# Optimization experiments

Measured on AMD Instinct MI355X. Metric: run time of the kernel, lower is better.

The kernel has to match this reference:

```python
import jax, jax.numpy as jnp
import numpy as np

B, N, K = 32, 64, 128          # batch, atoms per cell, channel width (128x0e + 128x1o)
R_MAX = 5.0
NUM_BESSEL = 8
P_CUT = 5                       # num_polynomial_cutoff
AVG_NEIGH = 16.0                # avg_num_neighbors
H_MLP = 512                     # hidden_dimensions_size, n_hidden_dimensions = 2
FEAT = 5 * K                    # ((num_interactions-1)*4 + 1) * 128 = 640


def silu(x):
    return x * jax.nn.sigmoid(x)


def _bessel_cutoff(r, mask):
    # Bessel radial basis * polynomial cutoff (MACE), masked on valid edges.
    n = jnp.arange(1, NUM_BESSEL + 1, dtype=r.dtype)
    rb = jnp.sqrt(2.0 / R_MAX) * jnp.sin(n * (jnp.pi / R_MAX) * r[..., None]) / r[..., None]
    u = r / R_MAX
    p = float(P_CUT)
    fc = 1.0 - 0.5 * (p + 1) * (p + 2) * u**P_CUT + p * (p + 2) * u**(P_CUT + 1) - 0.5 * p * (p + 1) * u**(P_CUT + 2)
    fc = fc * (u < 1.0)
    return rb * (fc * mask)[..., None]


def _sph(uvec):
    # Real spherical harmonics l=0,1,2 (component normalization), uvec: unit edge vectors.
    x, y, z = uvec[..., 0], uvec[..., 1], uvec[..., 2]
    s3, s5, s15 = 3.0**0.5, 5.0**0.5, 15.0**0.5
    Y0 = jnp.ones_like(x)[..., None]
    Y1 = jnp.stack([s3 * x, s3 * y, s3 * z], -1)
    Y2 = jnp.stack([s15 * x * y, s15 * y * z, 0.5 * s5 * (3 * z * z - 1.0),
                    s15 * x * z, 0.5 * s15 * (x * x - y * y)], -1)
    return Y0, Y1, Y2


def _radial_mlp(x, w0, b0, w1, b1, w2, b2, w3, b3):
    h = silu(x @ w0 + b0)
    h = silu(h @ w1 + b1)
    h = silu(h @ w2 + b2)
    return h @ w3 + b3


def setup_inputs() -> dict:
    key = jax.random.key(0)
    ks = jax.random.split(key, 32)
    f32 = jnp.float32

    def lin(k, fan_in, shape):
        return (jax.random.normal(k, shape, dtype=f32) / np.sqrt(fan_in)).astype(f32)

    inp = {
        "noisy_relative_positions": jax.random.uniform(ks[0], (B, N, 3), dtype=f32),
        "time": jax.random.uniform(ks[1], (B, 1), dtype=f32),
        "unit_cell": (11.0 * jnp.eye(3, dtype=f32) + 0.3 * jax.random.uniform(ks[2], (B, 3, 3), dtype=f32)),
        "w_embed": lin(ks[3], 1, (K,)),
        # interaction 1 radial MLP: 8 -> 64 -> 64 -> 64 -> 3*K (weights for l=0,1,2 paths)
        "r1_w0": lin(ks[4], NUM_BESSEL, (NUM_BESSEL, 64)), "r1_b0": jnp.zeros((64,), f32),
        "r1_w1": lin(ks[5], 64, (64, 64)), "r1_b1": jnp.zeros((64,), f32),
        "r1_w2": lin(ks[6], 64, (64, 64)), "r1_b2": jnp.zeros((64,), f32),
        "r1_w3": lin(ks[7], 64, (64, 3 * K)), "r1_b3": jnp.zeros((3 * K,), f32),
        "mix1_l0": lin(ks[8], K, (K, K)),
        "mix1_l1": lin(ks[9], K, (K, K)),
        "mix1_l2": lin(ks[10], K, (K, K)),
        # interaction 2 radial MLP: 8 -> 64 -> 64 -> 64 -> 2*K (paths 0e x 0e -> 0e, 1o x 1o -> 0e)
        "r2_w0": lin(ks[11], NUM_BESSEL, (NUM_BESSEL, 64)), "r2_b0": jnp.zeros((64,), f32),
        "r2_w1": lin(ks[12], 64, (64, 64)), "r2_b1": jnp.zeros((64,), f32),
        "r2_w2": lin(ks[13], 64, (64, 64)), "r2_b2": jnp.zeros((64,), f32),
        "r2_w3": lin(ks[14], 64, (64, 2 * K)), "r2_b3": jnp.zeros((2 * K,), f32),
        "mix2": lin(ks[15], K, (K, K)),
        # readout MLP: 641 -> 512 -> 512 -> 3
        "mlp_w0": lin(ks[16], FEAT + 1, (FEAT + 1, H_MLP)), "mlp_b0": jnp.zeros((H_MLP,), f32),
        "mlp_w1": lin(ks[17], H_MLP, (H_MLP, H_MLP)), "mlp_b1": jnp.zeros((H_MLP,), f32),
        "mlp_w2": lin(ks[18], H_MLP, (H_MLP, 3)), "mlp_b2": jnp.zeros((3,), f32),
    }
    return inp


def reference(noisy_relative_positions, time, unit_cell, w_embed,
              r1_w0, r1_b0, r1_w1, r1_b1, r1_w2, r1_b2, r1_w3, r1_b3,
              mix1_l0, mix1_l1, mix1_l2,
              r2_w0, r2_b0, r2_w1, r2_b1, r2_w2, r2_b2, r2_w3, r2_b3, mix2,
              mlp_w0, mlp_b0, mlp_w1, mlp_b1, mlp_w2, mlp_b2):
    frac = noisy_relative_positions                      # [B,N,3] fractional
    d = frac[:, :, None, :] - frac[:, None, :, :]        # [B,N,N,3]
    d = d - jnp.round(d)                                 # minimum-image PBC
    dc = jnp.einsum('bijc,bcd->bijd', d, unit_cell)      # cartesian displacements
    r = jnp.sqrt(jnp.maximum(jnp.sum(dc * dc, -1), 1e-12))
    mask = (r < R_MAX) & (~jnp.eye(N, dtype=bool))[None]
    r_safe = jnp.where(mask, r, 1.0)
    uvec = dc / r_safe[..., None] * mask[..., None]      # unit edge vectors (0 off-edge)

    rad = _bessel_cutoff(r_safe, mask)                   # [B,N,N,8]
    Y0, Y1, Y2 = _sph(uvec)                              # [B,N,N,1|3|5]

    h0 = jnp.broadcast_to(w_embed, (B, N, K))            # element embedding (single species)

    # ---- interaction 1: radial-weighted tensor product h_j (x) Y_l, scatter over j ----
    we = _radial_mlp(rad, r1_w0, r1_b0, r1_w1, r1_b1, r1_w2, r1_b2, r1_w3, r1_b3)
    we = we.reshape(B, N, N, 3, K) * mask[..., None, None]
    hj = h0[:, None, :, :]                               # sender features [B,1,N,K]
    msg0 = jnp.einsum('bijk,bijm->bimk', we[..., 0, :] * hj, Y0)[:, :, 0] / AVG_NEIGH  # [B,N,K]
    msg1 = jnp.einsum('bijk,bijm->bimk', we[..., 1, :] * hj, Y1) / AVG_NEIGH           # [B,N,3,K]
    msg2 = jnp.einsum('bijk,bijm->bimk', we[..., 2, :] * hj, Y2) / AVG_NEIGH           # [B,N,5,K]

    s1 = msg0 @ mix1_l0 + jnp.sum(msg2 * msg2, axis=2) @ mix1_l2   # scalars [B,N,K]
    v1 = jnp.einsum('bimk,kc->bimc', msg1, mix1_l1)                # vectors [B,N,3,K]
    h1 = silu(s1)

    # ---- interaction 2: scalar output from 0e x 0e and 1o x 1o -> 0e paths ----
    we2 = _radial_mlp(rad, r2_w0, r2_b0, r2_w1, r2_b1, r2_w2, r2_b2, r2_w3, r2_b3)
    we2 = we2.reshape(B, N, N, 2, K) * mask[..., None, None]
    msg_a = jnp.sum(we2[..., 0, :] * h1[:, None, :, :], axis=2)    # [B,N,K]
    inv = jnp.einsum('bijm,bjmk->bijk', Y1, v1)                    # Y1 . v1_j invariant
    msg_b = jnp.sum(we2[..., 1, :] * inv, axis=2)
    s2 = ((msg_a + msg_b) / AVG_NEIGH) @ mix2                      # [B,N,K]

    # node_feats: layer1 full irreps (128x0e + 128x1o -> 512) + layer2 scalars (128) = 640
    node_feats = jnp.concatenate([s1, v1.reshape(B, N, 3 * K), s2], axis=-1)

    t = jnp.broadcast_to(time[:, None, :], (B, N, 1))
    x = jnp.concatenate([node_feats, t], axis=-1)                  # [B,N,641]
    x = jax.nn.relu(x @ mlp_w0 + mlp_b0)
    x = jax.nn.relu(x @ mlp_w1 + mlp_b1)
    return x @ mlp_w2 + mlp_b2                                     # [B,N,3]
```

## Files before the change

kernel.cpp:

```cpp
#include <hip/hip_runtime.h>
#include <math.h>

#define B_ 32
#define N_ 64
#define K_ 128
#define NPAIR (B_*N_*N_)

typedef __attribute__((ext_vector_type(8))) short short8;
typedef __attribute__((ext_vector_type(8))) __bf16 bf16x8;
typedef __attribute__((ext_vector_type(4))) float floatx4;

__device__ __forceinline__ float silu_f(float x) {
    return x / (1.0f + expf(-x));
}
__device__ __forceinline__ float4 ld4(const float* p) { return *(const float4*)p; }

__device__ __forceinline__ short f2bf(float x) {
    union { float f; unsigned u; } v; v.f = x;
    unsigned r = (v.u + 0x7FFFu + ((v.u >> 16) & 1u)) >> 16;
    return (short)r;
}
__device__ __forceinline__ float bf2f(short s) {
    union { unsigned u; float f; } v;
    v.u = ((unsigned)(unsigned short)s) << 16;
    return v.f;
}
__device__ __forceinline__ bf16x8 ld_frag(const short* p) {
    short8 r = *(const short8*)p;
    return __builtin_bit_cast(bf16x8, r);
}

__global__ __launch_bounds__(256) void prep_kernel(
    const float* __restrict__ r1w1, const float* __restrict__ r1w2,
    const float* __restrict__ r2w1, const float* __restrict__ r2w2,
    const float* __restrict__ r2w3, const float* __restrict__ mw0,
    const float* __restrict__ mw1, short* __restrict__ dst)
{
    int idx = blockIdx.x * 256 + threadIdx.x;
    if (idx >= 655360) return;
    short v;
    if (idx < 4096) {
        int h = idx >> 6, k = idx & 63; v = f2bf(r1w1[k*64 + h]);
    } else if (idx < 8192) {
        int i = idx - 4096; int h = i >> 6, k = i & 63; v = f2bf(r1w2[k*64 + h]);
    } else if (idx < 12288) {
        int i = idx - 8192; int h = i >> 6, k = i & 63; v = f2bf(r2w1[k*64 + h]);
    } else if (idx < 16384) {
        int i = idx - 12288; int h = i >> 6, k = i & 63; v = f2bf(r2w2[k*64 + h]);
    } else if (idx < 32768) {
        int i = idx - 16384; int col = i >> 6, h = i & 63; v = f2bf(r2w3[h*256 + col]);
    } else if (idx < 393216) {
        int i = idx - 32768; int n = i / 704, k = i - n*704;
        v = (k < 641) ? f2bf(mw0[(size_t)k*512 + n]) : (short)0;
    } else {
        int i = idx - 393216; int n = i >> 9, k = i & 511;
        v = f2bf(mw1[(size_t)k*512 + n]);
    }
    dst[idx] = v;
}

__global__ __launch_bounds__(256) void geom_kernel(
    const float* __restrict__ pos, const float* __restrict__ cell,
    float* __restrict__ rad, float* __restrict__ Y1, float* __restrict__ Y2,
    float* __restrict__ maskf)
{
    int p = blockIdx.x * 256 + threadIdx.x;
    if (p >= NPAIR) return;
    int b = p >> 12;
    int ij = p & 4095;
    int i = ij >> 6, j = ij & 63;
    const float* pi = pos + (size_t)(b*N_ + i)*3;
    const float* pj = pos + (size_t)(b*N_ + j)*3;
    float d0 = pi[0]-pj[0], d1 = pi[1]-pj[1], d2 = pi[2]-pj[2];
    d0 -= rintf(d0); d1 -= rintf(d1); d2 -= rintf(d2);
    const float* C = cell + b*9;
    float dc0 = d0*C[0] + d1*C[3] + d2*C[6];
    float dc1 = d0*C[1] + d1*C[4] + d2*C[7];
    float dc2 = d0*C[2] + d1*C[5] + d2*C[8];
    float r2 = fmaxf(dc0*dc0 + dc1*dc1 + dc2*dc2, 1e-12f);
    float r = sqrtf(r2);
    bool m = (r < 5.0f) && (i != j);
    float mf = m ? 1.0f : 0.0f;
    float rs = m ? r : 1.0f;
    float inv_rs = 1.0f / rs;
    float x = dc0*inv_rs*mf, y = dc1*inv_rs*mf, z = dc2*inv_rs*mf;
    float u = r * 0.2f;
    float u2 = u*u, u4 = u2*u2, u5 = u4*u;
    float fc = 1.0f - 21.0f*u5 + 35.0f*u5*u - 15.0f*u5*u2;
    fc = (u < 1.0f) ? fc : 0.0f;
    float pref = 0.6324555320336759f * inv_rs * (fc * mf);
    float w = 0.6283185307179586f * rs;
    #pragma unroll
    for (int n = 1; n <= 8; n++)
        rad[(size_t)p*8 + (n-1)] = pref * sinf((float)n * w);
    const float s3  = 1.7320508075688772f;
    const float s5  = 2.23606797749979f;
    const float s15 = 3.872983346207417f;
    float* y1 = Y1 + (size_t)p*3;
    y1[0] = s3*x; y1[1] = s3*y; y1[2] = s3*z;
    float* y2 = Y2 + (size_t)p*5;
    y2[0] = s15*x*y;
    y2[1] = s15*y*z;
    y2[2] = 0.5f*s5*(3.0f*z*z - 1.0f);
    y2[3] = s15*x*z;
    y2[4] = 0.5f*s15*(x*x - y*y);
    maskf[p] = mf;
}

__device__ __forceinline__ void mfma_layer(
    const short* __restrict__ src, const short* __restrict__ WT,
    const float* __restrict__ bias, short* __restrict__ dst,
    int wv, int qd, int nn)
{
    floatx4 acc[4];
    #pragma unroll
    for (int tt = 0; tt < 4; tt++) acc[tt] = (floatx4){0.f, 0.f, 0.f, 0.f};
    #pragma unroll
    for (int ks = 0; ks < 64; ks += 32) {
        bf16x8 a = ld_frag(&src[(wv*16 + nn)*72 + ks + qd*8]);
        #pragma unroll
        for (int tt = 0; tt < 4; tt++) {
            bf16x8 b = ld_frag(&WT[(tt*16 + nn)*64 + ks + qd*8]);
            acc[tt] = __builtin_amdgcn_mfma_f32_16x16x32_bf16(a, b, acc[tt], 0, 0, 0);
        }
    }
    #pragma unroll
    for (int tt = 0; tt < 4; tt++) {
        int col = tt*16 + nn;
        float bv = bias[col];
        #pragma unroll
        for (int i = 0; i < 4; i++) {
            int row = wv*16 + qd*4 + i;
            dst[row*72 + col] = f2bf(silu_f(acc[tt][i] + bv));
        }
    }
}

__global__ __launch_bounds__(256) void pass1_kernel(
    const float* __restrict__ rad, const float* __restrict__ Y1g,
    const float* __restrict__ Y2g, const float* __restrict__ maskg,
    const float* __restrict__ wemb,
    const float* __restrict__ w0, const float* __restrict__ b0,
    const short* __restrict__ w1T, const float* __restrict__ b1,
    const short* __restrict__ w2T, const float* __restrict__ b2,
    const float* __restrict__ w3, const float* __restrict__ b3,
    const float* __restrict__ l0, const float* __restrict__ l1,
    const float* __restrict__ l2, const float* __restrict__ timeg,
    float* __restrict__ h1g, float* __restrict__ v1g, short* __restrict__ featsb)
{
    __shared__ float rad_s[512];
    __shared__ short actA[64*72];
    __shared__ short actB[64*72];
    __shared__ float Ym[9*64];
    __shared__ float G[9*64];
    __shared__ float SY[9];
    __shared__ float msg[9*128];
    __shared__ float q_s[128];
    int t = threadIdx.x;
    int wv = t >> 6, lane = t & 63, qd = lane >> 4, nn = lane & 15;
    int node = blockIdx.x;
    int b = node >> 6;
    size_t pbase = (size_t)node * 64;

    for (int idx = t; idx < 512; idx += 256) rad_s[idx] = rad[pbase*8 + idx];
    if (t < 64) {
        int j = t;
        float mf = maskg[pbase + j];
        Ym[j] = mf;
        #pragma unroll
        for (int m = 0; m < 3; m++) Ym[(1+m)*64 + j] = Y1g[(pbase+j)*3 + m] * mf;
        #pragma unroll
        for (int m = 0; m < 5; m++) Ym[(4+m)*64 + j] = Y2g[(pbase+j)*5 + m] * mf;
    }
    __syncthreads();

    for (int idx = t; idx < 4096; idx += 256) {
        int j = idx >> 6, h = idx & 63;
        float acc = b0[h];
        #pragma unroll
        for (int c = 0; c < 8; c++) acc += rad_s[j*8+c] * w0[c*64+h];
        actA[j*72 + h] = f2bf(silu_f(acc));
    }
    __syncthreads();
    mfma_layer(actA, w1T, b1, actB, wv, qd, nn);
    __syncthreads();
    mfma_layer(actB, w2T, b2, actA, wv, qd, nn);
    __syncthreads();

    if (t < 9) {
        float acc = 0.f;
        for (int j = 0; j < 64; j++) acc += Ym[t*64 + j];
        SY[t] = acc;
    }
    for (int idx = t; idx < 576; idx += 256) {
        int m = idx >> 6, h = idx & 63;
        float acc = 0.f;
        #pragma unroll 8
        for (int j = 0; j < 64; j++) acc += Ym[m*64 + j] * bf2f(actA[j*72 + h]);
        G[m*64 + h] = acc;
    }
    __syncthreads();

    for (int idx = t; idx < 1152; idx += 256) {
        int m = idx >> 7, k = idx & 127;
        int c = (m == 0) ? 0 : ((m < 4) ? 1 : 2);
        int col = c*128 + k;
        float acc = SY[m] * b3[col];
        #pragma unroll 8
        for (int h = 0; h < 64; h++) acc += G[m*64 + h] * w3[h*384 + col];
        msg[m*128 + k] = acc * wemb[k] * 0.0625f;
    }
    __syncthreads();

    if (t < 128) {
        int k = t;
        float acc = 0.f;
        #pragma unroll
        for (int m = 4; m < 9; m++) { float v = msg[m*128 + k]; acc += v*v; }
        q_s[k] = acc;
    }
    __syncthreads();

    for (int idx = t; idx < 512; idx += 256) {
        if (idx < 128) {
            int c = idx;
            float acc = 0.f;
            for (int k = 0; k < 128; k++)
                acc += msg[k]*l0[k*128 + c] + q_s[k]*l2[k*128 + c];
            featsb[(size_t)node*704 + c] = f2bf(acc);
            h1g[(size_t)node*128 + c] = silu_f(acc);
        } else {
            int vi = idx - 128;
            int m = vi >> 7, c = vi & 127;
            float acc = 0.f;
            for (int k = 0; k < 128; k++) acc += msg[(1+m)*128 + k]*l1[k*128 + c];
            v1g[(size_t)node*384 + m*128 + c] = acc;
            featsb[(size_t)node*704 + 128 + m*128 + c] = f2bf(acc);
        }
    }
    if (t == 0) featsb[(size_t)node*704 + 640] = f2bf(timeg[b]);
    if (t < 63) featsb[(size_t)node*704 + 641 + t] = 0;
}

__global__ __launch_bounds__(256) void pass2_kernel(
    const float* __restrict__ rad, const float* __restrict__ Y1g,
    const float* __restrict__ maskg,
    const float* __restrict__ w0, const float* __restrict__ b0,
    const short* __restrict__ w1T, const float* __restrict__ b1,
    const short* __restrict__ w2T, const float* __restrict__ b2,
    const short* __restrict__ w3T, const float* __restrict__ b3,
    const float* __restrict__ mix2,
    const float* __restrict__ h1g, const float* __restrict__ v1g,
    short* __restrict__ featsb)
{
    __shared__ float rad_s[512];
    __shared__ short actA[64*72];
    __shared__ short actB[64*72];
    __shared__ float Y1s[64*4];
    __shared__ float mask_s[64];
    __shared__ float msgab[128];
    int t = threadIdx.x;
    int wv = t >> 6, lane = t & 63, qd = lane >> 4, nn = lane & 15;
    int node = blockIdx.x;
    int b = node >> 6;
    size_t pbase = (size_t)node * 64;

    for (int idx = t; idx < 512; idx += 256) rad_s[idx] = rad[pbase*8 + idx];
    if (t < 64) {
        mask_s[t] = maskg[pbase + t];
        #pragma unroll
        for (int m = 0; m < 3; m++) Y1s[t*4 + m] = Y1g[(pbase+t)*3 + m];
    }
    if (t < 128) msgab[t] = 0.f;
    __syncthreads();

    for (int idx = t; idx < 4096; idx += 256) {
        int j = idx >> 6, h = idx & 63;
        float acc = b0[h];
        #pragma unroll
        for (int c = 0; c < 8; c++) acc += rad_s[j*8+c] * w0[c*64+h];
        actA[j*72 + h] = f2bf(silu_f(acc));
    }
    __syncthreads();
    mfma_layer(actA, w1T, b1, actB, wv, qd, nn);
    __syncthreads();
    mfma_layer(actB, w2T, b2, actA, wv, qd, nn);
    __syncthreads();

    for (int g = 0; g < 4; g++) {
        floatx4 acc[4];
        #pragma unroll
        for (int tt = 0; tt < 4; tt++) acc[tt] = (floatx4){0.f, 0.f, 0.f, 0.f};
        #pragma unroll
        for (int ks = 0; ks < 64; ks += 32) {
            bf16x8 a = ld_frag(&actA[(wv*16 + nn)*72 + ks + qd*8]);
            #pragma unroll
            for (int tt = 0; tt < 4; tt++) {
                int col0 = g*64 + tt*16;
                bf16x8 bb = ld_frag(&w3T[(col0 + nn)*64 + ks + qd*8]);
                acc[tt] = __builtin_amdgcn_mfma_f32_16x16x32_bf16(a, bb, acc[tt], 0, 0, 0);
            }
        }
        #pragma unroll
        for (int tt = 0; tt < 4; tt++) {
            int col = g*64 + tt*16 + nn;
            float bias = b3[col];
            int k = col & 127;
            float p = 0.f;
            if (col < 128) {
                #pragma unroll
                for (int i = 0; i < 4; i++) {
                    int j = wv*16 + qd*4 + i;
                    float we = (acc[tt][i] + bias) * mask_s[j];
                    p += we * h1g[((size_t)b*64 + j)*128 + k];
                }
            } else {
                #pragma unroll
                for (int i = 0; i < 4; i++) {
                    int j = wv*16 + qd*4 + i;
                    float we = (acc[tt][i] + bias) * mask_s[j];
                    const float* vb = &v1g[((size_t)b*64 + j)*384 + k];
                    float inv = Y1s[j*4+0]*vb[0] + Y1s[j*4+1]*vb[128] + Y1s[j*4+2]*vb[256];
                    p += we * inv;
                }
            }
            p += __shfl_xor(p, 16);
            p += __shfl_xor(p, 32);
            if (qd == 0) atomicAdd(&msgab[k], p);
        }
    }
    __syncthreads();

    if (t < 128) {
        int c = t;
        float acc = 0.f;
        for (int k = 0; k < 128; k++) acc += msgab[k] * mix2[k*128 + c];
        featsb[(size_t)node*704 + 512 + c] = f2bf(acc * 0.0625f);
    }
}

__global__ __launch_bounds__(256) void gemm_mfma_kernel(
    const short* __restrict__ A, int lda,
    const short* __restrict__ BT, int ldb, int K,
    const float* __restrict__ bias, short* __restrict__ Cout, int ldo)
{
    __shared__ short As[64*72];
    __shared__ short Bs[64*72];
    int t = threadIdx.x;
    int wv = t >> 6, lane = t & 63, qd = lane >> 4, nn = lane & 15;
    int m0 = blockIdx.x * 64, n0 = blockIdx.y * 64;
    floatx4 acc[4];
    #pragma unroll
    for (int tt = 0; tt < 4; tt++) acc[tt] = (floatx4){0.f, 0.f, 0.f, 0.f};

    for (int kc = 0; kc < K; kc += 64) {
        for (int s = t; s < 512; s += 256) {
            int j = s >> 3, kk = (s & 7) * 8;
            *(uint4*)&As[j*72 + kk] = *(const uint4*)&A[(size_t)(m0 + j)*lda + kc + kk];
            *(uint4*)&Bs[j*72 + kk] = *(const uint4*)&BT[(size_t)(n0 + j)*ldb + kc + kk];
        }
        __syncthreads();
        #pragma unroll
        for (int ks = 0; ks < 64; ks += 32) {
            bf16x8 a = ld_frag(&As[(wv*16 + nn)*72 + ks + qd*8]);
            #pragma unroll
            for (int tt = 0; tt < 4; tt++) {
                bf16x8 bb = ld_frag(&Bs[(tt*16 + nn)*72 + ks + qd*8]);
                acc[tt] = __builtin_amdgcn_mfma_f32_16x16x32_bf16(a, bb, acc[tt], 0, 0, 0);
            }
        }
        __syncthreads();
    }
    #pragma unroll
    for (int tt = 0; tt < 4; tt++) {
        int n = n0 + tt*16 + nn;
        float bv = bias[n];
        #pragma unroll
        for (int i = 0; i < 4; i++) {
            int m = m0 + wv*16 + qd*4 + i;
            Cout[(size_t)m*ldo + n] = f2bf(fmaxf(acc[tt][i] + bv, 0.f));
        }
    }
}

__global__ __launch_bounds__(64) void final3_kernel(
    const short* __restrict__ H, const float* __restrict__ w2,
    const float* __restrict__ b2, float* __restrict__ out)
{
    int node = blockIdx.x, lane = threadIdx.x;
    float a0 = 0.f, a1 = 0.f, a2 = 0.f;
    #pragma unroll
    for (int r = 0; r < 8; r++) {
        int k = r*64 + lane;
        float h = bf2f(H[(size_t)node*512 + k]);
        a0 += h * w2[k*3 + 0];
        a1 += h * w2[k*3 + 1];
        a2 += h * w2[k*3 + 2];
    }
    #pragma unroll
    for (int off = 32; off > 0; off >>= 1) {
        a0 += __shfl_down(a0, off);
        a1 += __shfl_down(a1, off);
        a2 += __shfl_down(a2, off);
    }
    if (lane == 0) {
        out[(size_t)node*3 + 0] = a0 + b2[0];
        out[(size_t)node*3 + 1] = a1 + b2[1];
        out[(size_t)node*3 + 2] = a2 + b2[2];
    }
}

extern "C" void kernel_launch(void* const* d_in, const int* in_sizes, int n_in,
                              void* d_out, int out_size, void* d_ws, size_t ws_size,
                              hipStream_t stream) {
    const float* pos   = (const float*)d_in[0];
    const float* timeg = (const float*)d_in[1];
    const float* cell  = (const float*)d_in[2];
    const float* wemb  = (const float*)d_in[3];
    const float* r1w0  = (const float*)d_in[4];
    const float* r1b0  = (const float*)d_in[5];
    const float* r1w1  = (const float*)d_in[6];
    const float* r1b1  = (const float*)d_in[7];
    const float* r1w2  = (const float*)d_in[8];
    const float* r1b2  = (const float*)d_in[9];
    const float* r1w3  = (const float*)d_in[10];
    const float* r1b3  = (const float*)d_in[11];
    const float* l0    = (const float*)d_in[12];
    const float* l1    = (const float*)d_in[13];
    const float* l2    = (const float*)d_in[14];
    const float* r2w0  = (const float*)d_in[15];
    const float* r2b0  = (const float*)d_in[16];
    const float* r2w1  = (const float*)d_in[17];
    const float* r2b1  = (const float*)d_in[18];
    const float* r2w2  = (const float*)d_in[19];
    const float* r2b2  = (const float*)d_in[20];
    const float* r2w3  = (const float*)d_in[21];
    const float* r2b3  = (const float*)d_in[22];
    const float* mix2  = (const float*)d_in[23];
    const float* mw0   = (const float*)d_in[24];
    const float* mb0   = (const float*)d_in[25];
    const float* mw1   = (const float*)d_in[26];
    const float* mb1   = (const float*)d_in[27];
    const float* mw2   = (const float*)d_in[28];
    const float* mb2   = (const float*)d_in[29];

    float* ws    = (float*)d_ws;
    float* rad   = ws;
    float* Y1    = rad   + (size_t)NPAIR*8;
    float* Y2    = Y1    + (size_t)NPAIR*3;
    float* maskf = Y2    + (size_t)NPAIR*5;
    float* h1    = maskf + (size_t)NPAIR;
    float* v1    = h1    + (size_t)B_*N_*K_;
    short* featsb = (short*)(v1 + (size_t)B_*N_*3*K_);
    short* prep  = featsb + (size_t)2048*704;
    short* w1T_1 = prep;
    short* w2T_1 = prep + 4096;
    short* w1T_2 = prep + 8192;
    short* w2T_2 = prep + 12288;
    short* w3T_2 = prep + 16384;
    short* wT0   = prep + 32768;
    short* wT1   = prep + 393216;
    short* h0bb = (short*)rad;
    short* h1bb = (short*)Y2;

    prep_kernel<<<(655360 + 255)/256, 256, 0, stream>>>(
        r1w1, r1w2, r2w1, r2w2, r2w3, mw0, mw1, prep);
    geom_kernel<<<NPAIR/256, 256, 0, stream>>>(pos, cell, rad, Y1, Y2, maskf);
    pass1_kernel<<<B_*N_, 256, 0, stream>>>(rad, Y1, Y2, maskf, wemb,
        r1w0, r1b0, w1T_1, r1b1, w2T_1, r1b2, r1w3, r1b3, l0, l1, l2, timeg,
        h1, v1, featsb);
    pass2_kernel<<<B_*N_, 256, 0, stream>>>(rad, Y1, maskf,
        r2w0, r2b0, w1T_2, r2b1, w2T_2, r2b2, w3T_2, r2b3, mix2, h1, v1, featsb);
    dim3 g0(32, 8);
    gemm_mfma_kernel<<<g0, 256, 0, stream>>>(featsb, 704, wT0, 704, 704, mb0, h0bb, 512);
    gemm_mfma_kernel<<<g0, 256, 0, stream>>>(h0bb, 512, wT1, 512, 512, mb1, h1bb, 512);
    final3_kernel<<<B_*N_, 64, 0, stream>>>(h1bb, mw2, mb2, (float*)d_out);
}
```

Measured before the change: 286.0 us.

## Move remaining radial-MLP and mixing stages of both interaction passes onto bf16 MFMA

The first radial layer, the Y·h contraction, the w3 projection and the l0/l1/l2 channel mixing in pass1 now run as bf16 MFMA tiles instead of scalar FP32 loops. pass2 stages h1 and the Y1·v1 invariant into shared memory as bf16 rather than re-reading global memory per MFMA output. The prep kernel adds transposed bf16 copies of w0, w3 (with wemb and 1/16 folded in) and the stacked mixing weights, and the geometry kernel computes the Bessel sines with a Chebyshev recurrence and vector stores. Shared memory is packed into one aliased pool. The extra bf16 rounding of intermediates adds numerical error.

```diff
diff --git a/kernel.cpp b/kernel.cpp
--- a/kernel.cpp
+++ b/kernel.cpp
@@ -31,30 +31,50 @@
 }
 
 __global__ __launch_bounds__(256) void prep_kernel(
-    const float* __restrict__ r1w1, const float* __restrict__ r1w2,
-    const float* __restrict__ r2w1, const float* __restrict__ r2w2,
-    const float* __restrict__ r2w3, const float* __restrict__ mw0,
-    const float* __restrict__ mw1, short* __restrict__ dst)
+    const float* __restrict__ r1w0, const float* __restrict__ r1w1,
+    const float* __restrict__ r1w2, const float* __restrict__ r1w3,
+    const float* __restrict__ r2w0, const float* __restrict__ r2w1,
+    const float* __restrict__ r2w2, const float* __restrict__ r2w3,
+    const float* __restrict__ mw0, const float* __restrict__ mw1,
+    const float* __restrict__ wemb,
+    const float* __restrict__ l0, const float* __restrict__ l1,
+    const float* __restrict__ l2, short* __restrict__ dst)
 {
     int idx = blockIdx.x * 256 + threadIdx.x;
-    if (idx >= 655360) return;
+    if (idx >= 733184) return;
     short v;
     if (idx < 4096) {
-        int h = idx >> 6, k = idx & 63; v = f2bf(r1w1[k*64 + h]);
+        int n = idx >> 6, k = idx & 63; v = f2bf(r1w1[k*64 + n]);
     } else if (idx < 8192) {
-        int i = idx - 4096; int h = i >> 6, k = i & 63; v = f2bf(r1w2[k*64 + h]);
+        int i = idx - 4096; int n = i >> 6, k = i & 63; v = f2bf(r1w2[k*64 + n]);
     } else if (idx < 12288) {
-        int i = idx - 8192; int h = i >> 6, k = i & 63; v = f2bf(r2w1[k*64 + h]);
+        int i = idx - 8192; int n = i >> 6, k = i & 63; v = f2bf(r2w1[k*64 + n]);
     } else if (idx < 16384) {
-        int i = idx - 12288; int h = i >> 6, k = i & 63; v = f2bf(r2w2[k*64 + h]);
+        int i = idx - 12288; int n = i >> 6, k = i & 63; v = f2bf(r2w2[k*64 + n]);
     } else if (idx < 32768) {
         int i = idx - 16384; int col = i >> 6, h = i & 63; v = f2bf(r2w3[h*256 + col]);
     } else if (idx < 393216) {
         int i = idx - 32768; int n = i / 704, k = i - n*704;
         v = (k < 641) ? f2bf(mw0[(size_t)k*512 + n]) : (short)0;
-    } else {
+    } else if (idx < 655360) {
         int i = idx - 393216; int n = i >> 9, k = i & 511;
         v = f2bf(mw1[(size_t)k*512 + n]);
+    } else if (idx < 657408) {
+        int i = idx - 655360; int n = i >> 5, k = i & 31;
+        v = (k < 8) ? f2bf(r1w0[k*64 + n]) : (short)0;
+    } else if (idx < 659456) {
+        int i = idx - 657408; int n = i >> 5, k = i & 31;
+        v = (k < 8) ? f2bf(r2w0[k*64 + n]) : (short)0;
+    } else if (idx < 684032) {
+        int i = idx - 659456; int col = i >> 6, h = i & 63;
+        v = f2bf(r1w3[h*384 + col] * wemb[col & 127] * 0.0625f);
+    } else {
+        int i = idx - 684032; int n = i / 384, k = i - n*384;
+        float f;
+        if (k < 128)       f = l0[k*128 + n];
+        else if (k < 256)  f = l2[(k-128)*128 + n];
+        else               f = l1[(k-256)*128 + n];
+        v = f2bf(f);
     }
     dst[idx] = v;
 }
@@ -90,9 +110,20 @@
     fc = (u < 1.0f) ? fc : 0.0f;
     float pref = 0.6324555320336759f * inv_rs * (fc * mf);
     float w = 0.6283185307179586f * rs;
-    #pragma unroll
-    for (int n = 1; n <= 8; n++)
-        rad[(size_t)p*8 + (n-1)] = pref * sinf((float)n * w);
+    float sw = sinf(w), cw = cosf(w);
+    float c2 = 2.0f * cw;
+    float rr[8];
+    float sp = 0.f, s = sw;
+    #pragma unroll
+    for (int n = 0; n < 8; n++) {
+        rr[n] = pref * s;
+        float ns = c2*s - sp;
+        sp = s; s = ns;
+    }
+    float4 v0 = {rr[0], rr[1], rr[2], rr[3]};
+    float4 v1 = {rr[4], rr[5], rr[6], rr[7]};
+    *(float4*)&rad[(size_t)p*8]     = v0;
+    *(float4*)&rad[(size_t)p*8 + 4] = v1;
     const float s3  = 1.7320508075688772f;
     const float s5  = 2.23606797749979f;
     const float s15 = 3.872983346207417f;
@@ -107,7 +138,8 @@
     maskf[p] = mf;
 }
 
-__device__ __forceinline__ void mfma_layer(
+template<bool TRANSPOSE_OUT>
+__device__ __forceinline__ void mfma_layer_t(
     const short* __restrict__ src, const short* __restrict__ WT,
     const float* __restrict__ bias, short* __restrict__ dst,
     int wv, int qd, int nn)
@@ -131,7 +163,30 @@
         #pragma unroll
         for (int i = 0; i < 4; i++) {
             int row = wv*16 + qd*4 + i;
-            dst[row*72 + col] = f2bf(silu_f(acc[tt][i] + bv));
+            short val = f2bf(silu_f(acc[tt][i] + bv));
+            if (TRANSPOSE_OUT) dst[col*72 + row] = val;
+            else               dst[row*72 + col] = val;
+        }
+    }
+}
+
+__device__ __forceinline__ void mfma_layer0(
+    const short* __restrict__ radB, const short* __restrict__ w0T,
+    const float* __restrict__ bias, short* __restrict__ dst,
+    int wv, int qd, int nn)
+{
+    bf16x8 a = ld_frag(&radB[(wv*16 + nn)*40 + qd*8]);
+    #pragma unroll
+    for (int tt = 0; tt < 4; tt++) {
+        floatx4 acc = (floatx4){0.f, 0.f, 0.f, 0.f};
+        bf16x8 b = ld_frag(&w0T[(tt*16 + nn)*32 + qd*8]);
+        acc = __builtin_amdgcn_mfma_f32_16x16x32_bf16(a, b, acc, 0, 0, 0);
+        int col = tt*16 + nn;
+        float bv = bias[col];
+        #pragma unroll
+        for (int i = 0; i < 4; i++) {
+            int row = wv*16 + qd*4 + i;
+            dst[row*72 + col] = f2bf(silu_f(acc[i] + bv));
         }
     }
 }
@@ -140,102 +195,141 @@
     const float* __restrict__ rad, const float* __restrict__ Y1g,
     const float* __restrict__ Y2g, const float* __restrict__ maskg,
     const float* __restrict__ wemb,
-    const float* __restrict__ w0, const float* __restrict__ b0,
+    const short* __restrict__ w0T, const float* __restrict__ b0,
     const short* __restrict__ w1T, const float* __restrict__ b1,
     const short* __restrict__ w2T, const float* __restrict__ b2,
-    const float* __restrict__ w3, const float* __restrict__ b3,
-    const float* __restrict__ l0, const float* __restrict__ l1,
-    const float* __restrict__ l2, const float* __restrict__ timeg,
+    const short* __restrict__ w3T, const float* __restrict__ b3,
+    const short* __restrict__ lT, const float* __restrict__ timeg,
     float* __restrict__ h1g, float* __restrict__ v1g, short* __restrict__ featsb)
 {
-    __shared__ float rad_s[512];
-    __shared__ short actA[64*72];
-    __shared__ short actB[64*72];
-    __shared__ float Ym[9*64];
-    __shared__ float G[9*64];
-    __shared__ float SY[9];
-    __shared__ float msg[9*128];
-    __shared__ float q_s[128];
+    __shared__ __align__(16) char pool[32832];
+    short* radB = (short*)pool;
+    short* hcT  = (short*)pool;
+    short* actA = (short*)(pool + 9216);
+    short* actB = (short*)(pool + 18432);
+    short* A2   = (short*)(pool + 9216);
+    float* msgF = (float*)(pool + 21760);
+    short* YmB  = (short*)(pool + 27648);
+    short* GB   = (short*)(pool + 29952);
+    float* qF   = (float*)(pool + 32256);
+    float* SY   = (float*)(pool + 32768);
+
     int t = threadIdx.x;
     int wv = t >> 6, lane = t & 63, qd = lane >> 4, nn = lane & 15;
     int node = blockIdx.x;
     int b = node >> 6;
     size_t pbase = (size_t)node * 64;
 
-    for (int idx = t; idx < 512; idx += 256) rad_s[idx] = rad[pbase*8 + idx];
+    for (int idx = t; idx < 2560; idx += 256) {
+        int j = idx / 40, c = idx - j*40;
+        radB[idx] = (c < 8) ? f2bf(rad[pbase*8 + j*8 + c]) : (short)0;
+    }
+    for (int idx = t; idx < 1152; idx += 256) YmB[idx] = 0;
+    __syncthreads();
+
     if (t < 64) {
         int j = t;
         float mf = maskg[pbase + j];
-        Ym[j] = mf;
-        #pragma unroll
-        for (int m = 0; m < 3; m++) Ym[(1+m)*64 + j] = Y1g[(pbase+j)*3 + m] * mf;
-        #pragma unroll
-        for (int m = 0; m < 5; m++) Ym[(4+m)*64 + j] = Y2g[(pbase+j)*5 + m] * mf;
-    }
-    __syncthreads();
-
-    for (int idx = t; idx < 4096; idx += 256) {
-        int j = idx >> 6, h = idx & 63;
-        float acc = b0[h];
-        #pragma unroll
-        for (int c = 0; c < 8; c++) acc += rad_s[j*8+c] * w0[c*64+h];
-        actA[j*72 + h] = f2bf(silu_f(acc));
-    }
-    __syncthreads();
-    mfma_layer(actA, w1T, b1, actB, wv, qd, nn);
-    __syncthreads();
-    mfma_layer(actB, w2T, b2, actA, wv, qd, nn);
-    __syncthreads();
-
-    if (t < 9) {
+        YmB[j] = f2bf(mf);
+        #pragma unroll
+        for (int m = 0; m < 3; m++) YmB[(1+m)*72 + j] = f2bf(Y1g[(pbase+j)*3 + m] * mf);
+        #pragma unroll
+        for (int m = 0; m < 5; m++) YmB[(4+m)*72 + j] = f2bf(Y2g[(pbase+j)*5 + m] * mf);
+    }
+    mfma_layer0(radB, w0T, b0, actA, wv, qd, nn);
+    __syncthreads();
+
+    mfma_layer_t<false>(actA, w1T, b1, actB, wv, qd, nn);
+    __syncthreads();
+    mfma_layer_t<true >(actB, w2T, b2, hcT,  wv, qd, nn);
+    __syncthreads();
+
+    if (t < 16) {
         float acc = 0.f;
-        for (int j = 0; j < 64; j++) acc += Ym[t*64 + j];
+        if (t < 9) for (int j = 0; j < 64; j++) acc += bf2f(YmB[t*72 + j]);
         SY[t] = acc;
     }
-    for (int idx = t; idx < 576; idx += 256) {
-        int m = idx >> 6, h = idx & 63;
+    {
+        floatx4 accG = (floatx4){0.f, 0.f, 0.f, 0.f};
+        #pragma unroll
+        for (int ks = 0; ks < 64; ks += 32) {
+            bf16x8 a = ld_frag(&YmB[nn*72 + ks + qd*8]);
+            bf16x8 bfr = ld_frag(&hcT[(wv*16 + nn)*72 + ks + qd*8]);
+            accG = __builtin_amdgcn_mfma_f32_16x16x32_bf16(a, bfr, accG, 0, 0, 0);
+        }
+        #pragma unroll
+        for (int i = 0; i < 4; i++)
+            GB[(qd*4 + i)*72 + wv*16 + nn] = f2bf(accG[i]);
+    }
+    __syncthreads();
+
+    {
+        bf16x8 a0f = ld_frag(&GB[nn*72 + 0  + qd*8]);
+        bf16x8 a1f = ld_frag(&GB[nn*72 + 32 + qd*8]);
+        #pragma unroll
+        for (int tl = 0; tl < 6; tl++) {
+            int col0 = (wv*6 + tl)*16;
+            floatx4 acc = (floatx4){0.f, 0.f, 0.f, 0.f};
+            bf16x8 b0f = ld_frag(&w3T[(col0 + nn)*64 + 0  + qd*8]);
+            bf16x8 b1f = ld_frag(&w3T[(col0 + nn)*64 + 32 + qd*8]);
+            acc = __builtin_amdgcn_mfma_f32_16x16x32_bf16(a0f, b0f, acc, 0, 0, 0);
+            acc = __builtin_amdgcn_mfma_f32_16x16x32_bf16(a1f, b1f, acc, 0, 0, 0);
+            int col = col0 + nn;
+            int csec = col >> 7, k = col & 127;
+            #pragma unroll
+            for (int i = 0; i < 4; i++) {
+                int m = qd*4 + i;
+                bool valid = (csec == 0) ? (m == 0)
+                           : (csec == 1) ? (m >= 1 && m <= 3)
+                                         : (m >= 4 && m <= 8);
+                if (valid)
+                    msgF[m*128 + k] = acc[i] + SY[m]*b3[col]*wemb[k]*0.0625f;
+            }
+        }
+    }
+    __syncthreads();
+
+    if (t < 128) {
         float acc = 0.f;
-        #pragma unroll 8
-        for (int j = 0; j < 64; j++) acc += Ym[m*64 + j] * bf2f(actA[j*72 + h]);
-        G[m*64 + h] = acc;
-    }
-    __syncthreads();
-
-    for (int idx = t; idx < 1152; idx += 256) {
-        int m = idx >> 7, k = idx & 127;
-        int c = (m == 0) ? 0 : ((m < 4) ? 1 : 2);
-        int col = c*128 + k;
-        float acc = SY[m] * b3[col];
-        #pragma unroll 8
-        for (int h = 0; h < 64; h++) acc += G[m*64 + h] * w3[h*384 + col];
-        msg[m*128 + k] = acc * wemb[k] * 0.0625f;
-    }
-    __syncthreads();
-
-    if (t < 128) {
-        int k = t;
-        float acc = 0.f;
-        #pragma unroll
-        for (int m = 4; m < 9; m++) { float v = msg[m*128 + k]; acc += v*v; }
-        q_s[k] = acc;
-    }
-    __syncthreads();
-
-    for (int idx = t; idx < 512; idx += 256) {
-        if (idx < 128) {
-            int c = idx;
-            float acc = 0.f;
-            for (int k = 0; k < 128; k++)
-                acc += msg[k]*l0[k*128 + c] + q_s[k]*l2[k*128 + c];
-            featsb[(size_t)node*704 + c] = f2bf(acc);
-            h1g[(size_t)node*128 + c] = silu_f(acc);
-        } else {
-            int vi = idx - 128;
-            int m = vi >> 7, c = vi & 127;
-            float acc = 0.f;
-            for (int k = 0; k < 128; k++) acc += msg[(1+m)*128 + k]*l1[k*128 + c];
-            v1g[(size_t)node*384 + m*128 + c] = acc;
-            featsb[(size_t)node*704 + 128 + m*128 + c] = f2bf(acc);
+        #pragma unroll
+        for (int m = 4; m < 9; m++) { float v = msgF[m*128 + t]; acc += v*v; }
+        qF[t] = acc;
+    }
+    __syncthreads();
+
+    for (int idx = t; idx < 6272; idx += 256) A2[idx] = 0;
+    __syncthreads();
+    {
+        int idx = t;
+        A2[idx] = (idx < 128) ? f2bf(msgF[idx]) : f2bf(qF[idx - 128]);
+        if (t < 128) {
+            #pragma unroll
+            for (int m = 1; m <= 3; m++)
+                A2[m*392 + 256 + t] = f2bf(msgF[m*128 + t]);
+        }
+    }
+    __syncthreads();
+
+    #pragma unroll
+    for (int tt = 0; tt < 2; tt++) {
+        int col = (wv*2 + tt)*16 + nn;
+        floatx4 acc = (floatx4){0.f, 0.f, 0.f, 0.f};
+        #pragma unroll
+        for (int ks = 0; ks < 384; ks += 32) {
+            bf16x8 a = ld_frag(&A2[nn*392 + ks + qd*8]);
+            bf16x8 bfr = ld_frag(&lT[(size_t)col*384 + ks + qd*8]);
+            acc = __builtin_amdgcn_mfma_f32_16x16x32_bf16(a, bfr, acc, 0, 0, 0);
+        }
+        if (qd == 0) {
+            float s1 = acc[0];
+            featsb[(size_t)node*704 + col] = f2bf(s1);
+            h1g[(size_t)node*128 + col] = silu_f(s1);
+            #pragma unroll
+            for (int i = 1; i < 4; i++) {
+                float v = acc[i];
+                v1g[(size_t)node*384 + (i-1)*128 + col] = v;
+                featsb[(size_t)node*704 + 128 + (i-1)*128 + col] = f2bf(v);
+            }
         }
     }
     if (t == 0) featsb[(size_t)node*704 + 640] = f2bf(timeg[b]);
@@ -245,7 +339,7 @@
 __global__ __launch_bounds__(256) void pass2_kernel(
     const float* __restrict__ rad, const float* __restrict__ Y1g,
     const float* __restrict__ maskg,
-    const float* __restrict__ w0, const float* __restrict__ b0,
+    const short* __restrict__ w0T, const float* __restrict__ b0,
     const short* __restrict__ w1T, const float* __restrict__ b1,
     const short* __restrict__ w2T, const float* __restrict__ b2,
     const short* __restrict__ w3T, const float* __restrict__ b3,
@@ -253,19 +347,27 @@
     const float* __restrict__ h1g, const float* __restrict__ v1g,
     short* __restrict__ featsb)
 {
-    __shared__ float rad_s[512];
-    __shared__ short actA[64*72];
-    __shared__ short actB[64*72];
-    __shared__ float Y1s[64*4];
-    __shared__ float mask_s[64];
-    __shared__ float msgab[128];
+    __shared__ __align__(16) char pool[46848];
+    short* radB  = (short*)pool;
+    short* hc    = (short*)pool;
+    short* actA  = (short*)(pool + 9216);
+    short* actB  = (short*)(pool + 18432);
+    short* h1B   = (short*)(pool + 9216);
+    short* invB  = (short*)(pool + 27648);
+    float* Y1s   = (float*)(pool + 45056);
+    float* mask_s= (float*)(pool + 46080);
+    float* msgab = (float*)(pool + 46336);
+
     int t = threadIdx.x;
     int wv = t >> 6, lane = t & 63, qd = lane >> 4, nn = lane & 15;
     int node = blockIdx.x;
     int b = node >> 6;
     size_t pbase = (size_t)node * 64;
 
-    for (int idx = t; idx < 512; idx += 256) rad_s[idx] = rad[pbase*8 + idx];
+    for (int idx = t; idx < 2560; idx += 256) {
+        int j = idx / 40, c = idx - j*40;
+        radB[idx] = (c < 8) ? f2bf(rad[pbase*8 + j*8 + c]) : (short)0;
+    }
     if (t < 64) {
         mask_s[t] = maskg[pbase + t];
         #pragma unroll
@@ -274,68 +376,67 @@
     if (t < 128) msgab[t] = 0.f;
     __syncthreads();
 
-    for (int idx = t; idx < 4096; idx += 256) {
-        int j = idx >> 6, h = idx & 63;
-        float acc = b0[h];
-        #pragma unroll
-        for (int c = 0; c < 8; c++) acc += rad_s[j*8+c] * w0[c*64+h];
-        actA[j*72 + h] = f2bf(silu_f(acc));
-    }
-    __syncthreads();
-    mfma_layer(actA, w1T, b1, actB, wv, qd, nn);
-    __syncthreads();
-    mfma_layer(actB, w2T, b2, actA, wv, qd, nn);
-    __syncthreads();
-
-    for (int g = 0; g < 4; g++) {
-        floatx4 acc[4];
-        #pragma unroll
-        for (int tt = 0; tt < 4; tt++) acc[tt] = (floatx4){0.f, 0.f, 0.f, 0.f};
-        #pragma unroll
-        for (int ks = 0; ks < 64; ks += 32) {
-            bf16x8 a = ld_frag(&actA[(wv*16 + nn)*72 + ks + qd*8]);
+    mfma_layer0(radB, w0T, b0, actA, wv, qd, nn);
+    __syncthreads();
+    mfma_layer_t<false>(actA, w1T, b1, actB, wv, qd, nn);
+    __syncthreads();
+    mfma_layer_t<false>(actB, w2T, b2, hc, wv, qd, nn);
+    __syncthreads();
+
+    for (int idx = t; idx < 2048; idx += 256) {
+        int j = idx >> 5, kq = (idx & 31)*4;
+        size_t gj = (size_t)b*64 + j;
+        float4 hv = ld4(&h1g[gj*128 + kq]);
+        h1B[j*136 + kq + 0] = f2bf(hv.x);
+        h1B[j*136 + kq + 1] = f2bf(hv.y);
+        h1B[j*136 + kq + 2] = f2bf(hv.z);
+        h1B[j*136 + kq + 3] = f2bf(hv.w);
+        const float* vb = &v1g[gj*384 + kq];
+        float4 vx = ld4(vb), vy = ld4(vb + 128), vz = ld4(vb + 256);
+        float yx = Y1s[j*4+0], yy = Y1s[j*4+1], yz = Y1s[j*4+2];
+        invB[j*136 + kq + 0] = f2bf(yx*vx.x + yy*vy.x + yz*vz.x);
+        invB[j*136 + kq + 1] = f2bf(yx*vx.y + yy*vy.y + yz*vz.y);
+        invB[j*136 + kq + 2] = f2bf(yx*vx.z + yy*vy.z + yz*vz.z);
+        invB[j*136 + kq + 3] = f2bf(yx*vx.w + yy*vy.w + yz*vz.w);
+    }
+    __syncthreads();
+
+    {
+        bf16x8 aA = ld_frag(&hc[(wv*16 + nn)*72 + 0  + qd*8]);
+        bf16x8 aB = ld_frag(&hc[(wv*16 + nn)*72 + 32 + qd*8]);
+        #pragma unroll
+        for (int g = 0; g < 4; g++) {
             #pragma unroll
             for (int tt = 0; tt < 4; tt++) {
                 int col0 = g*64 + tt*16;
-                bf16x8 bb = ld_frag(&w3T[(col0 + nn)*64 + ks + qd*8]);
-                acc[tt] = __builtin_amdgcn_mfma_f32_16x16x32_bf16(a, bb, acc[tt], 0, 0, 0);
-            }
-        }
-        #pragma unroll
-        for (int tt = 0; tt < 4; tt++) {
-            int col = g*64 + tt*16 + nn;
-            float bias = b3[col];
-            int k = col & 127;
-            float p = 0.f;
-            if (col < 128) {
+                floatx4 acc = (floatx4){0.f, 0.f, 0.f, 0.f};
+                bf16x8 b0f = ld_frag(&w3T[(col0 + nn)*64 + 0  + qd*8]);
+                bf16x8 b1f = ld_frag(&w3T[(col0 + nn)*64 + 32 + qd*8]);
+                acc = __builtin_amdgcn_mfma_f32_16x16x32_bf16(aA, b0f, acc, 0, 0, 0);
+                acc = __builtin_amdgcn_mfma_f32_16x16x32_bf16(aB, b1f, acc, 0, 0, 0);
+                int col = col0 + nn;
+                int k = col & 127;
+                float bias = b3[col];
+                const short* src = (col < 128) ? h1B : invB;
+                float p = 0.f;
                 #pragma unroll
                 for (int i = 0; i < 4; i++) {
                     int j = wv*16 + qd*4 + i;
-                    float we = (acc[tt][i] + bias) * mask_s[j];
-                    p += we * h1g[((size_t)b*64 + j)*128 + k];
+                    float we = (acc[i] + bias) * mask_s[j];
+                    p += we * bf2f(src[j*136 + k]);
                 }
-            } else {
-                #pragma unroll
-                for (int i = 0; i < 4; i++) {
-                    int j = wv*16 + qd*4 + i;
-                    float we = (acc[tt][i] + bias) * mask_s[j];
-                    const float* vb = &v1g[((size_t)b*64 + j)*384 + k];
-                    float inv = Y1s[j*4+0]*vb[0] + Y1s[j*4+1]*vb[128] + Y1s[j*4+2]*vb[256];
-                    p += we * inv;
-                }
+                p += __shfl_xor(p, 16);
+                p += __shfl_xor(p, 32);
+                if (qd == 0) atomicAdd(&msgab[k], p);
             }
-            p += __shfl_xor(p, 16);
-            p += __shfl_xor(p, 32);
-            if (qd == 0) atomicAdd(&msgab[k], p);
         }
     }
     __syncthreads();
 
     if (t < 128) {
-        int c = t;
         float acc = 0.f;
-        for (int k = 0; k < 128; k++) acc += msgab[k] * mix2[k*128 + c];
-        featsb[(size_t)node*704 + 512 + c] = f2bf(acc * 0.0625f);
+        for (int k = 0; k < 128; k++) acc += msgab[k] * mix2[k*128 + t];
+        featsb[(size_t)node*704 + 512 + t] = f2bf(acc * 0.0625f);
     }
 }
 
@@ -460,17 +561,22 @@
     short* w3T_2 = prep + 16384;
     short* wT0   = prep + 32768;
     short* wT1   = prep + 393216;
+    short* w0T_1 = prep + 655360;
+    short* w0T_2 = prep + 657408;
+    short* w3T_1 = prep + 659456;
+    short* lT    = prep + 684032;
     short* h0bb = (short*)rad;
     short* h1bb = (short*)Y2;
 
-    prep_kernel<<<(655360 + 255)/256, 256, 0, stream>>>(
-        r1w1, r1w2, r2w1, r2w2, r2w3, mw0, mw1, prep);
+    prep_kernel<<<(733184 + 255)/256, 256, 0, stream>>>(
+        r1w0, r1w1, r1w2, r1w3, r2w0, r2w1, r2w2, r2w3, mw0, mw1,
+        wemb, l0, l1, l2, prep);
     geom_kernel<<<NPAIR/256, 256, 0, stream>>>(pos, cell, rad, Y1, Y2, maskf);
     pass1_kernel<<<B_*N_, 256, 0, stream>>>(rad, Y1, Y2, maskf, wemb,
-        r1w0, r1b0, w1T_1, r1b1, w2T_1, r1b2, r1w3, r1b3, l0, l1, l2, timeg,
+        w0T_1, r1b0, w1T_1, r1b1, w2T_1, r1b2, w3T_1, r1b3, lT, timeg,
         h1, v1, featsb);
     pass2_kernel<<<B_*N_, 256, 0, stream>>>(rad, Y1, maskf,
-        r2w0, r2b0, w1T_2, r2b1, w2T_2, r2b2, w3T_2, r2b3, mix2, h1, v1, featsb);
+        w0T_2, r2b0, w1T_2, r2b1, w2T_2, r2b2, w3T_2, r2b3, mix2, h1, v1, featsb);
     dim3 g0(32, 8);
     gemm_mfma_kernel<<<g0, 256, 0, stream>>>(featsb, 704, wT0, 704, 704, mb0, h0bb, 512);
     gemm_mfma_kernel<<<g0, 256, 0, stream>>>(h0bb, 512, wT1, 512, 512, mb1, h1bb, 512);
```

Measured after the change: 292.2 us. 1.02x slower.
